# Kernel optimization log

Measured on AMD Instinct MI355X. Metric: run time of the kernel, lower is better.

## Reference

```python
import jax, jax.numpy as jnp
import numpy as np

LOG2 = 0.6931471805599453
GAMMA = 10.0
NUM_KERNELS = 301
N_LAYERS = 3


def ssp(v):
    # ShiftedSoftplus: softplus(x) - log(2)
    return jax.nn.softplus(v) - jnp.asarray(LOG2, v.dtype)


def setup_inputs() -> dict:
    key = jax.random.key(0)
    ks = jax.random.split(key, 20)
    N, F, K, L, V = 512, 128, NUM_KERNELS, N_LAYERS, 100
    s = 0.05
    return {
        "x": jax.random.randint(ks[0], (N,), 0, V),
        "r": jax.random.uniform(ks[1], (N, 3), dtype=jnp.float32) * 10.0,
        "emb": jax.random.normal(ks[2], (V, F), dtype=jnp.float32),
        "aw_W": jax.random.normal(ks[3], (L, F, F), dtype=jnp.float32) * s,
        "aw_b": jax.random.normal(ks[4], (L, F), dtype=jnp.float32) * s,
        "cf_W1": jax.random.normal(ks[5], (L, K, F), dtype=jnp.float32) * s,
        "cf_b1": jax.random.normal(ks[6], (L, F), dtype=jnp.float32) * s,
        "cf_W2": jax.random.normal(ks[7], (L, F, F), dtype=jnp.float32) * s,
        "cf_b2": jax.random.normal(ks[8], (L, F), dtype=jnp.float32) * s,
        "n_W1": jax.random.normal(ks[9], (L, F, F), dtype=jnp.float32) * s,
        "n_b1": jax.random.normal(ks[10], (L, F), dtype=jnp.float32) * s,
        "n_W2": jax.random.normal(ks[11], (L, F, F), dtype=jnp.float32) * s,
        "n_b2": jax.random.normal(ks[12], (L, F), dtype=jnp.float32) * s,
        "out_W1": jax.random.normal(ks[13], (F, 32), dtype=jnp.float32) * s,
        "out_b1": jax.random.normal(ks[14], (32,), dtype=jnp.float32) * s,
        "out_W2": jax.random.normal(ks[15], (32, 1), dtype=jnp.float32) * s,
        "out_b2": jax.random.normal(ks[16], (1,), dtype=jnp.float32) * s,
    }


def reference(x, r, emb, aw_W, aw_b, cf_W1, cf_b1, cf_W2, cf_b2,
              n_W1, n_b1, n_W2, n_b2, out_W1, out_b1, out_W2, out_b2):
    centers = jnp.linspace(0.0, 30.0, NUM_KERNELS, dtype=r.dtype)  # [K]
    # pairwise distances (torch.cdist, p=2) with safe sqrt at the diagonal
    diff = r[:, None, :] - r[None, :, :]                 # [N,N,3]
    d2 = jnp.sum(diff * diff, axis=-1)                   # [N,N]
    mask = d2 > 0
    d = jnp.where(mask, jnp.sqrt(jnp.where(mask, d2, 1.0)), 0.0)

    h = emb[x]                                           # [N,F]
    for l in range(N_LAYERS):
        o = h @ aw_W[l] + aw_b[l]                        # atom-wise linear
        # Gaussian RBF expansion: [N,N,K]
        e = jnp.exp(-GAMMA * jnp.square(d[..., None] - centers))
        # filter-generating MLP: [N,N,F]
        w = ssp(e @ cf_W1[l] + cf_b1[l])
        w = ssp(w @ cf_W2[l] + cf_b2[l])
        # continuous-filter conv: o[i,k] = sum_j x[j,k] * w[i,j,k]
        c = jnp.einsum('jk,ijk->ik', o, w)
        c = ssp(c @ n_W1[l] + n_b1[l]) @ n_W2[l] + n_b2[l]
        h = h + c
    out = ssp(h @ out_W1 + out_b1) @ out_W2 + out_b2     # [N,1]
    # AdaptiveAvgPool1d(1) on a 2D [N,1] tensor is identity over L=1
    return out.reshape(-1)
```

## Files before the change

### kernel.cpp

```cpp
#include <hip/hip_runtime.h>
#include <hip/hip_fp16.h>
#include <math.h>

#define N_ATOMS 512
#define F_DIM   128
#define K_RBF   301
#define NLAYER  3
#define GAMMA_C 10.0f
#define LOG2_C  0.6931471805599453f

#define TAB_H     0.01f
#define TAB_INVH  100.0f
#define TAB_ROWS  1768
#define RPB       8
#define NGROUPS   (TAB_ROWS / RPB)
#define NTASKS    (NGROUPS * NLAYER)
#define NBBLK2    ((NTASKS + 1) / 2)
#define ROW_BYTES 512

#define JSPLIT  8
#define JPB     (N_ATOMS / JSPLIT)

__device__ __forceinline__ float ssp(float x) {
    float ax = fabsf(x);
    return fmaxf(x, 0.0f) + log1pf(expf(-ax)) - LOG2_C;
}
__device__ __forceinline__ __half2 u2h2(unsigned u) {
    union { unsigned u; __half2 h; } c; c.u = u; return c.h;
}
__device__ __forceinline__ unsigned h22u(__half2 h) {
    union { unsigned u; __half2 h; } c; c.h = h; return c.u;
}

__global__ void __launch_bounds__(256)
prep_build(const int* __restrict__ x, const float* __restrict__ r,
           const float* __restrict__ emb,
           const float* __restrict__ aw_W, const float* __restrict__ aw_b,
           const float* __restrict__ cf_W1, const float* __restrict__ cf_b1,
           const float* __restrict__ cf_W2, const float* __restrict__ cf_b2,
           uint2* __restrict__ dpk, float* __restrict__ h,
           unsigned* __restrict__ opk, uint2* __restrict__ ptab) {
    __shared__ float hs[F_DIM];
    __shared__ float os[F_DIM];
    __shared__ float red2[2 * F_DIM];
    __shared__ float e_s[2][RPB + 1][34];
    __shared__ float w1_s[2][F_DIM][12];

    if (blockIdx.x < N_ATOMS) {
        int i = blockIdx.x;
        int t = threadIdx.x;
        float rx = r[i * 3 + 0], ry = r[i * 3 + 1], rz = r[i * 3 + 2];
        if (t < F_DIM) {
            float hv = emb[x[i] * F_DIM + t];
            h[i * F_DIM + t] = hv;
            hs[t] = hv;
        }
        for (int j = t; j < N_ATOMS; j += 256) {
            float dx = rx - r[j * 3 + 0];
            float dy = ry - r[j * 3 + 1];
            float dz = rz - r[j * 3 + 2];
            float d  = sqrtf(dx * dx + dy * dy + dz * dz);
            float xb = d * TAB_INVH;
            int   b  = ::min((int)xb, TAB_ROWS - 2);
            float fr = xb - (float)b;
            __half fh = __float2half(fr);
            dpk[i * N_ATOMS + j] = make_uint2((unsigned)b * ROW_BYTES,
                                              h22u(__halves2half2(fh, fh)));
        }
        __syncthreads();
        {
            int q = t >> 7, f = t & 127;
            float a = 0.0f;
            int g0 = q * 64;
            for (int g = 0; g < 64; ++g)
                a = fmaf(hs[g0 + g], aw_W[(g0 + g) * F_DIM + f], a);
            red2[q * F_DIM + f] = a;
        }
        __syncthreads();
        if (t < F_DIM) os[t] = red2[t] + red2[F_DIM + t] + aw_b[t];
        __syncthreads();
        if (t < F_DIM / 2)
            opk[i * 64 + t] = h22u(__halves2half2(__float2half(os[2 * t]),
                                                  __float2half(os[2 * t + 1])));
        return;
    }

    int u = threadIdx.x >> 7;
    int f = threadIdx.x & 127;
    int task = (blockIdx.x - N_ATOMS) * 2 + u;
    bool valid = task < NTASKS;
    task = valid ? task : NTASKS - 1;
    int l    = task / NGROUPS;
    int row0 = (task % NGROUPS) * RPB;

    float dlo = row0 * TAB_H;
    float dhi = (row0 + RPB) * TAB_H;
    int k0 = ::max(0, (int)ceilf((dlo - 1.45f) * 10.0f));
    int k1 = ::min(K_RBF - 1, (int)floorf((dhi + 1.45f) * 10.0f));
    int kw = k1 - k0 + 1;

    for (int idx = f; idx < (RPB + 1) * kw; idx += F_DIM) {
        int rr = idx / kw, kk = idx % kw;
        float dv = (row0 + rr) * TAB_H;
        float tt = dv - 0.1f * (float)(k0 + kk);
        e_s[u][rr][kk] = expf(-GAMMA_C * tt * tt);
    }
    __syncthreads();

    const float* W1 = cf_W1 + l * K_RBF * F_DIM;
    float b1v = cf_b1[l * F_DIM + f];
    float acc[RPB + 1];
#pragma unroll
    for (int rr = 0; rr <= RPB; ++rr) acc[rr] = b1v;
    for (int kk = 0; kk < kw; ++kk) {
        float w1v = W1[(k0 + kk) * F_DIM + f];
#pragma unroll
        for (int rr = 0; rr <= RPB; ++rr) acc[rr] = fmaf(e_s[u][rr][kk], w1v, acc[rr]);
    }
#pragma unroll
    for (int rr = 0; rr <= RPB; ++rr) w1_s[u][f][rr] = ssp(acc[rr]);
    __syncthreads();

    const float* W2 = cf_W2 + l * F_DIM * F_DIM;
    float b2v = cf_b2[l * F_DIM + f];
    float acc2[RPB + 1];
#pragma unroll
    for (int rr = 0; rr <= RPB; ++rr) acc2[rr] = b2v;
    for (int g = 0; g < F_DIM; ++g) {
        float w2v = W2[g * F_DIM + f];
        float4 wa = *(const float4*)&w1_s[u][g][0];
        float4 wb = *(const float4*)&w1_s[u][g][4];
        float  wc = w1_s[u][g][8];
        acc2[0] = fmaf(wa.x, w2v, acc2[0]);
        acc2[1] = fmaf(wa.y, w2v, acc2[1]);
        acc2[2] = fmaf(wa.z, w2v, acc2[2]);
        acc2[3] = fmaf(wa.w, w2v, acc2[3]);
        acc2[4] = fmaf(wb.x, w2v, acc2[4]);
        acc2[5] = fmaf(wb.y, w2v, acc2[5]);
        acc2[6] = fmaf(wb.z, w2v, acc2[6]);
        acc2[7] = fmaf(wb.w, w2v, acc2[7]);
        acc2[8] = fmaf(wc,   w2v, acc2[8]);
    }
    float o9[RPB + 1];
#pragma unroll
    for (int rr = 0; rr <= RPB; ++rr) o9[rr] = ssp(acc2[rr]);

    if (valid) {
        int p = f >> 1;
        bool odd = (f & 1);
#pragma unroll
        for (int rr = 0; rr < RPB; ++rr) {
            float t0 = o9[rr];
            float dt = o9[rr + 1] - o9[rr];
            float ot0 = __shfl_xor(t0, 1, 64);
            float odt = __shfl_xor(dt, 1, 64);
            if (!odd) {
                uint2 v = make_uint2(
                    h22u(__halves2half2(__float2half(t0), __float2half(ot0))),
                    h22u(__halves2half2(__float2half(dt), __float2half(odt))));
                ptab[((size_t)l * TAB_ROWS + row0 + rr) * 64 + p] = v;
            }
        }
    }
}

__global__ void __launch_bounds__(256, 8)
conv_kernel(const uint2* __restrict__ dpk, const unsigned* __restrict__ opk_in,
            const uint2* __restrict__ ptab, float* __restrict__ c_part, int l) {
    int bid = blockIdx.x;
    int i  = bid >> 3;
    int qs = bid & 7;
    int t  = threadIdx.x;
    int p2 = t & 31;
    int jc = t >> 5;

    __shared__ __align__(16) uint2 ds[JPB];
    __shared__ __align__(16) float redbuf[8 * 32 * 4];

    if (t < JPB) ds[t] = dpk[i * N_ATOMS + qs * JPB + t];
    __syncthreads();

    const char*  T  = (const char*)(ptab + (size_t)l * TAB_ROWS * 64) + p2 * 16;
    const uint2* ob = (const uint2*)opk_in + p2 + (size_t)(qs * JPB) * 32;

    int j0 = jc * 8;
    uint2 e[8];
#pragma unroll
    for (int k2 = 0; k2 < 4; ++k2) {
        uint4 w = *(const uint4*)&ds[j0 + 2 * k2];
        e[2 * k2]     = make_uint2(w.x, w.y);
        e[2 * k2 + 1] = make_uint2(w.z, w.w);
    }

    float4 acc = make_float4(0.0f, 0.0f, 0.0f, 0.0f);
#pragma unroll
    for (int b = 0; b < 2; ++b) {
        uint4 tv[4]; uint2 oh[4];
#pragma unroll
        for (int k = 0; k < 4; ++k) {
            tv[k] = *(const uint4*)(T + e[b * 4 + k].x);
            oh[k] = ob[(j0 + b * 4 + k) * 32];
        }
#pragma unroll
        for (int k = 0; k < 4; ++k) {
            __half2 fr2 = u2h2(e[b * 4 + k].y);
            __half2 wa = __hfma2(fr2, u2h2(tv[k].y), u2h2(tv[k].x));
            __half2 wb = __hfma2(fr2, u2h2(tv[k].w), u2h2(tv[k].z));
            __half2 oa  = u2h2(oh[k].x);
            __half2 obh = u2h2(oh[k].y);
            acc.x = fmaf(__half2float(__low2half(wa)),  __half2float(__low2half(oa)),  acc.x);
            acc.y = fmaf(__half2float(__high2half(wa)), __half2float(__high2half(oa)), acc.y);
            acc.z = fmaf(__half2float(__low2half(wb)),  __half2float(__low2half(obh)), acc.z);
            acc.w = fmaf(__half2float(__high2half(wb)), __half2float(__high2half(obh)), acc.w);
        }
    }
    *(float4*)&redbuf[(jc * 32 + p2) * 4] = acc;
    __syncthreads();
    if (t < 32) {
        float4 s = *(const float4*)&redbuf[t * 4];
#pragma unroll
        for (int g = 1; g < 8; ++g) {
            float4 v = *(const float4*)&redbuf[(g * 32 + t) * 4];
            s.x += v.x; s.y += v.y; s.z += v.z; s.w += v.w;
        }
        *(float4*)&c_part[((size_t)(i * JSPLIT + qs)) * F_DIM + 4 * t] = s;
    }
}

__global__ void __launch_bounds__(256)
node_kernel(const float* __restrict__ c_part,
            const float* __restrict__ n_W1, const float* __restrict__ n_b1,
            const float* __restrict__ n_W2, const float* __restrict__ n_b2,
            float* __restrict__ h,
            const float* __restrict__ aw_W, const float* __restrict__ aw_b,
            unsigned* __restrict__ opk_out,
            const float* __restrict__ oW1, const float* __restrict__ ob1,
            const float* __restrict__ oW2, const float* __restrict__ ob2,
            float* __restrict__ out, int l) {
    int i = blockIdx.x;
    int t = threadIdx.x;

    __shared__ __align__(16) float cs[F_DIM];
    __shared__ __align__(16) float t1s[F_DIM];
    __shared__ __align__(16) float hs[F_DIM];
    __shared__ __align__(16) float redbuf[2 * F_DIM];

    if (t < F_DIM) {
        const float* cp = c_part + (size_t)i * JSPLIT * F_DIM + t;
        float s = 0.0f;
#pragma unroll
        for (int k = 0; k < JSPLIT; ++k) s += cp[k * F_DIM];
        cs[t] = s;
        hs[t] = h[i * F_DIM + t];
    }
    __syncthreads();

    {
        int q = t >> 7, f = t & 127;
        const float* W1 = n_W1 + l * F_DIM * F_DIM;
        float a = 0.0f;
        int g0 = q * 64;
        for (int g = 0; g < 64; ++g) a = fmaf(cs[g0 + g], W1[(g0 + g) * F_DIM + f], a);
        redbuf[q * F_DIM + f] = a;
    }
    __syncthreads();
    if (t < F_DIM)
        t1s[t] = ssp(redbuf[t] + redbuf[F_DIM + t] + n_b1[l * F_DIM + t]);
    __syncthreads();

    {
        int q = t >> 7, f = t & 127;
        const float* W2 = n_W2 + l * F_DIM * F_DIM;
        float a = 0.0f;
        int g0 = q * 64;
        for (int g = 0; g < 64; ++g) a = fmaf(t1s[g0 + g], W2[(g0 + g) * F_DIM + f], a);
        redbuf[q * F_DIM + f] = a;
    }
    __syncthreads();
    if (t < F_DIM) {
        float hv = hs[t] + redbuf[t] + redbuf[F_DIM + t] + n_b2[l * F_DIM + t];
        hs[t] = hv;
        if (l < NLAYER - 1) h[i * F_DIM + t] = hv;
    }
    __syncthreads();

    if (l < NLAYER - 1) {
        {
            int q = t >> 7, f = t & 127;
            const float* W = aw_W + (l + 1) * F_DIM * F_DIM;
            float a = 0.0f;
            int g0 = q * 64;
            for (int g = 0; g < 64; ++g) a = fmaf(hs[g0 + g], W[(g0 + g) * F_DIM + f], a);
            redbuf[q * F_DIM + f] = a;
        }
        __syncthreads();
        if (t < F_DIM) {
            t1s[t] = redbuf[t] + redbuf[F_DIM + t] + aw_b[(l + 1) * F_DIM + t];
        }
        __syncthreads();
        if (t < F_DIM / 2)
            opk_out[i * 64 + t] = h22u(__halves2half2(__float2half(t1s[2 * t]),
                                                      __float2half(t1s[2 * t + 1])));
    } else {
        {
            int q = t >> 5, f = t & 31;
            float a = 0.0f;
            int g0 = q * 16;
            for (int g = 0; g < 16; ++g) a = fmaf(hs[g0 + g], oW1[(g0 + g) * 32 + f], a);
            redbuf[q * 32 + f] = a;
        }
        __syncthreads();
        float val = 0.0f;
        if (t < 32) {
            float a = ob1[t];
#pragma unroll
            for (int q = 0; q < 8; ++q) a += redbuf[q * 32 + t];
            val = ssp(a) * oW2[t];
        }
#pragma unroll
        for (int off = 16; off > 0; off >>= 1) val += __shfl_xor(val, off, 64);
        if (t == 0) out[i] = val + ob2[0];
    }
}

extern "C" void kernel_launch(void* const* d_in, const int* in_sizes, int n_in,
                              void* d_out, int out_size, void* d_ws, size_t ws_size,
                              hipStream_t stream) {
    const int*   x     = (const int*)  d_in[0];
    const float* r     = (const float*)d_in[1];
    const float* emb   = (const float*)d_in[2];
    const float* aw_W  = (const float*)d_in[3];
    const float* aw_b  = (const float*)d_in[4];
    const float* cf_W1 = (const float*)d_in[5];
    const float* cf_b1 = (const float*)d_in[6];
    const float* cf_W2 = (const float*)d_in[7];
    const float* cf_b2 = (const float*)d_in[8];
    const float* n_W1  = (const float*)d_in[9];
    const float* n_b1  = (const float*)d_in[10];
    const float* n_W2  = (const float*)d_in[11];
    const float* n_b2  = (const float*)d_in[12];
    const float* oW1   = (const float*)d_in[13];
    const float* ob1   = (const float*)d_in[14];
    const float* oW2   = (const float*)d_in[15];
    const float* ob2   = (const float*)d_in[16];
    float* out = (float*)d_out;

    char* ws = (char*)d_ws;
    uint2*    dpk    = (uint2*)ws;    ws += (size_t)N_ATOMS * N_ATOMS * 8;
    float*    h      = (float*)ws;    ws += (size_t)N_ATOMS * F_DIM * 4;
    unsigned* opkA   = (unsigned*)ws; ws += (size_t)N_ATOMS * (F_DIM / 2) * 4;
    unsigned* opkB   = (unsigned*)ws; ws += (size_t)N_ATOMS * (F_DIM / 2) * 4;
    uint2*    ptab   = (uint2*)ws;    ws += (size_t)NLAYER * TAB_ROWS * 64 * 8;
    float*    c_part = (float*)ws;

    prep_build<<<N_ATOMS + NBBLK2, 256, 0, stream>>>(
        x, r, emb, aw_W, aw_b, cf_W1, cf_b1, cf_W2, cf_b2, dpk, h, opkA, ptab);
    for (int l = 0; l < NLAYER; ++l) {
        unsigned* oin  = (l & 1) ? opkB : opkA;
        unsigned* oout = (l & 1) ? opkA : opkB;
        conv_kernel<<<N_ATOMS * JSPLIT, 256, 0, stream>>>(dpk, oin, ptab, c_part, l);
        node_kernel<<<N_ATOMS, 256, 0, stream>>>(
            c_part, n_W1, n_b1, n_W2, n_b2, h, aw_W, aw_b, oout,
            oW1, ob1, oW2, ob2, out, l);
    }
}
```

Baseline: 160.4 us.

## Widen conv per-thread feature slice to 8 and halve j-split blocks

The conv kernel now has each thread cover 8 features using 32-byte table loads and 16-byte o loads, instead of 4 features with 16-byte and 8-byte loads. Each block handles 128 neighbors j (JSPLIT 4) with 16 j-groups, and the final reduction runs per feature over 16 partial sums. This halves the number of blocks and partial-sum rows, so the node kernel sums only 4 partials, and it should cut per-block setup and reduction overhead. The costs are fewer blocks, a lower occupancy hint, and more registers per thread.

```diff
diff --git a/kernel.cpp b/kernel.cpp
--- a/kernel.cpp
+++ b/kernel.cpp
@@ -18,7 +18,7 @@
 #define NBBLK2    ((NTASKS + 1) / 2)
 #define ROW_BYTES 512
 
-#define JSPLIT  8
+#define JSPLIT  4
 #define JPB     (N_ATOMS / JSPLIT)
 
 __device__ __forceinline__ float ssp(float x) {
@@ -164,66 +164,72 @@
     }
 }
 
-__global__ void __launch_bounds__(256, 8)
+__global__ void __launch_bounds__(256, 4)
 conv_kernel(const uint2* __restrict__ dpk, const unsigned* __restrict__ opk_in,
             const uint2* __restrict__ ptab, float* __restrict__ c_part, int l) {
     int bid = blockIdx.x;
-    int i  = bid >> 3;
-    int qs = bid & 7;
+    int i  = bid >> 2;
+    int qs = bid & 3;
     int t  = threadIdx.x;
-    int p2 = t & 31;
-    int jc = t >> 5;
+    int p1 = t & 15;
+    int jg = t >> 4;
 
     __shared__ __align__(16) uint2 ds[JPB];
-    __shared__ __align__(16) float redbuf[8 * 32 * 4];
+    __shared__ __align__(16) float redbuf[16 * F_DIM];
 
     if (t < JPB) ds[t] = dpk[i * N_ATOMS + qs * JPB + t];
     __syncthreads();
 
-    const char*  T  = (const char*)(ptab + (size_t)l * TAB_ROWS * 64) + p2 * 16;
-    const uint2* ob = (const uint2*)opk_in + p2 + (size_t)(qs * JPB) * 32;
-
-    int j0 = jc * 8;
-    uint2 e[8];
-#pragma unroll
-    for (int k2 = 0; k2 < 4; ++k2) {
-        uint4 w = *(const uint4*)&ds[j0 + 2 * k2];
-        e[2 * k2]     = make_uint2(w.x, w.y);
-        e[2 * k2 + 1] = make_uint2(w.z, w.w);
-    }
-
-    float4 acc = make_float4(0.0f, 0.0f, 0.0f, 0.0f);
-#pragma unroll
-    for (int b = 0; b < 2; ++b) {
-        uint4 tv[4]; uint2 oh[4];
-#pragma unroll
-        for (int k = 0; k < 4; ++k) {
-            tv[k] = *(const uint4*)(T + e[b * 4 + k].x);
-            oh[k] = ob[(j0 + b * 4 + k) * 32];
-        }
-#pragma unroll
-        for (int k = 0; k < 4; ++k) {
-            __half2 fr2 = u2h2(e[b * 4 + k].y);
-            __half2 wa = __hfma2(fr2, u2h2(tv[k].y), u2h2(tv[k].x));
-            __half2 wb = __hfma2(fr2, u2h2(tv[k].w), u2h2(tv[k].z));
-            __half2 oa  = u2h2(oh[k].x);
-            __half2 obh = u2h2(oh[k].y);
-            acc.x = fmaf(__half2float(__low2half(wa)),  __half2float(__low2half(oa)),  acc.x);
-            acc.y = fmaf(__half2float(__high2half(wa)), __half2float(__high2half(oa)), acc.y);
-            acc.z = fmaf(__half2float(__low2half(wb)),  __half2float(__low2half(obh)), acc.z);
-            acc.w = fmaf(__half2float(__high2half(wb)), __half2float(__high2half(obh)), acc.w);
-        }
-    }
-    *(float4*)&redbuf[(jc * 32 + p2) * 4] = acc;
-    __syncthreads();
-    if (t < 32) {
-        float4 s = *(const float4*)&redbuf[t * 4];
-#pragma unroll
-        for (int g = 1; g < 8; ++g) {
-            float4 v = *(const float4*)&redbuf[(g * 32 + t) * 4];
-            s.x += v.x; s.y += v.y; s.z += v.z; s.w += v.w;
-        }
-        *(float4*)&c_part[((size_t)(i * JSPLIT + qs)) * F_DIM + 4 * t] = s;
+    const char*     Tbase = (const char*)(ptab + (size_t)l * TAB_ROWS * 64) + p1 * 32;
+    const unsigned* ov    = opk_in + (size_t)(qs * JPB) * 64 + 4 * p1;
+
+    float acc[8] = {0.f, 0.f, 0.f, 0.f, 0.f, 0.f, 0.f, 0.f};
+    int j0 = jg * 8;
+
+#define CONV8(ee, ta, tb, oh)                                                   \
+    {                                                                           \
+        __half2 fr2 = u2h2((ee).y);                                             \
+        __half2 w0 = __hfma2(fr2, u2h2((ta).y), u2h2((ta).x));                  \
+        __half2 w1 = __hfma2(fr2, u2h2((ta).w), u2h2((ta).z));                  \
+        __half2 w2 = __hfma2(fr2, u2h2((tb).y), u2h2((tb).x));                  \
+        __half2 w3 = __hfma2(fr2, u2h2((tb).w), u2h2((tb).z));                  \
+        __half2 o0 = u2h2((oh).x), o1 = u2h2((oh).y);                           \
+        __half2 o2 = u2h2((oh).z), o3 = u2h2((oh).w);                           \
+        acc[0] = fmaf(__half2float(__low2half(w0)),  __half2float(__low2half(o0)),  acc[0]); \
+        acc[1] = fmaf(__half2float(__high2half(w0)), __half2float(__high2half(o0)), acc[1]); \
+        acc[2] = fmaf(__half2float(__low2half(w1)),  __half2float(__low2half(o1)),  acc[2]); \
+        acc[3] = fmaf(__half2float(__high2half(w1)), __half2float(__high2half(o1)), acc[3]); \
+        acc[4] = fmaf(__half2float(__low2half(w2)),  __half2float(__low2half(o2)),  acc[4]); \
+        acc[5] = fmaf(__half2float(__high2half(w2)), __half2float(__high2half(o2)), acc[5]); \
+        acc[6] = fmaf(__half2float(__low2half(w3)),  __half2float(__low2half(o3)),  acc[6]); \
+        acc[7] = fmaf(__half2float(__high2half(w3)), __half2float(__high2half(o3)), acc[7]); \
+    }
+
+#pragma unroll
+    for (int jj = 0; jj < 8; jj += 2) {
+        uint4 w = *(const uint4*)&ds[j0 + jj];
+        uint2 eA = make_uint2(w.x, w.y), eB = make_uint2(w.z, w.w);
+        const char* TA = Tbase + eA.x;
+        const char* TB = Tbase + eB.x;
+        uint4 taA = *(const uint4*)TA;
+        uint4 tbA = *(const uint4*)(TA + 16);
+        uint4 taB = *(const uint4*)TB;
+        uint4 tbB = *(const uint4*)(TB + 16);
+        uint4 ohA = *(const uint4*)(ov + (size_t)(j0 + jj) * 64);
+        uint4 ohB = *(const uint4*)(ov + (size_t)(j0 + jj + 1) * 64);
+        CONV8(eA, taA, tbA, ohA)
+        CONV8(eB, taB, tbB, ohB)
+    }
+#undef CONV8
+
+    *(float4*)&redbuf[jg * F_DIM + 8 * p1]     = make_float4(acc[0], acc[1], acc[2], acc[3]);
+    *(float4*)&redbuf[jg * F_DIM + 8 * p1 + 4] = make_float4(acc[4], acc[5], acc[6], acc[7]);
+    __syncthreads();
+    if (t < F_DIM) {
+        float s = 0.0f;
+#pragma unroll
+        for (int g = 0; g < 16; ++g) s += redbuf[g * F_DIM + t];
+        c_part[((size_t)(i * JSPLIT + qs)) * F_DIM + t] = s;
     }
 }
 
@@ -247,10 +253,7 @@
 
     if (t < F_DIM) {
         const float* cp = c_part + (size_t)i * JSPLIT * F_DIM + t;
-        float s = 0.0f;
-#pragma unroll
-        for (int k = 0; k < JSPLIT; ++k) s += cp[k * F_DIM];
-        cs[t] = s;
+        cs[t] = (cp[0] + cp[F_DIM]) + (cp[2 * F_DIM] + cp[3 * F_DIM]);
         hs[t] = h[i * F_DIM + t];
     }
     __syncthreads();
```

New measurement: 158.7 us. About the same (-1.1%).
